# Performance work log

Hardware: AMD Instinct MI355X
Metric: run time of the kernel (lower is better)

## Reference

```python
import jax, jax.numpy as jnp
import numpy as np

B, V, C, M, CM, D, OUT = 16, 16, 64, 32, 16, 128, 600
VOCAB = {"cond": 4000, "proc": 2000, "drug": 600, "lab_item": 700, "lab_value": 2000, "inj_item": 400, "inj_value": 2000}


def _gru(x, Wih, Whh, bih, bhh):
    """Batch-first torch-style GRU. x: [N,T,D] -> (outputs [N,T,D], h_T [N,D])."""
    Dh = Whh.shape[1]

    def step(h, xt):
        gi = xt @ Wih.T + bih
        gh = h @ Whh.T + bhh
        ir, iz, ig = jnp.split(gi, 3, axis=-1)
        hr, hz, hg = jnp.split(gh, 3, axis=-1)
        r = jax.nn.sigmoid(ir + hr)
        z = jax.nn.sigmoid(iz + hz)
        n = jnp.tanh(ig + r * hg)
        h = (1.0 - z) * n + z * h
        return h, h

    h0 = jnp.zeros((x.shape[0], Dh), x.dtype)
    hT, ys = jax.lax.scan(step, h0, jnp.swapaxes(x, 0, 1))
    return jnp.swapaxes(ys, 0, 1), hT


def _hetero_mp(feats, Wself, Wmsg):
    """Heterogeneous message passing over node types on the fully-connected
    monitor<->visit-feature bipartite pattern: each node type combines a self
    transform with a transformed mean of the other node types, then ReLU.
    feats: list of [N,D]; Wself/Wmsg: [T,D,D]."""
    stacked = jnp.stack(feats)  # [T,N,D]
    total = jnp.sum(stacked, axis=0)
    T = stacked.shape[0]
    outs = []
    for t in range(T):
        others = (total - stacked[t]) / (T - 1)
        outs.append(jax.nn.relu(stacked[t] @ Wself[t] + others @ Wmsg[t]))
    return outs


def _forward(codes_cond, codes_proc, codes_drug, codes_lab_item, codes_lab_value,
             codes_inj_item, codes_inj_value, weight, age,
             emb_cond, emb_proc, emb_drug, emb_lab_item, emb_lab_value,
             emb_inj_item, emb_inj_value,
             mgru_Wih, mgru_Whh, mgru_bih, mgru_bhh,
             vgru_Wih, vgru_Whh, vgru_bih, vgru_bhh,
             gnn_Wself, gnn_Wmsg,
             fc_weight_W, fc_weight_b, fc_age_W, fc_age_b,
             fc_patient_W, fc_patient_b):
    # ---- visit-event features: embedding lookup + sum-pool over codes ----
    vis = {}
    for k, codes, emb in (("cond", codes_cond, emb_cond),
                          ("proc", codes_proc, emb_proc),
                          ("drug", codes_drug, emb_drug)):
        vis[k] = jnp.sum(emb[codes], axis=2)  # [B,V,D]
    visit_keys = ("cond", "proc", "drug")

    # ---- monitor-event pairs: (item * value) embeddings, GNN, two-level GRU ----
    pairs = (
        (codes_lab_item, codes_lab_value, emb_lab_item, emb_lab_value, "lab_item", (0, 2, 3, 4)),
        (codes_inj_item, codes_inj_value, emb_inj_item, emb_inj_value, "inj_item", (1, 2, 3, 4)),
    )
    hid = {}
    for p, (ci, cv, ei, ev, ikey, gidx) in enumerate(pairs):
        mon = jnp.sum(ei[ci] * ev[cv], axis=3)  # [B,V,M,D]
        feats = [mon.reshape(-1, D)]  # monitor node type, [B*V*M, D]
        for k in visit_keys:  # visit features repeated across monitors
            feats.append(jnp.broadcast_to(vis[k][:, :, None, :], (B, V, M, D)).reshape(-1, D))
        outs = _hetero_mp(feats, gnn_Wself[p], gnn_Wmsg[p])
        for t, k in enumerate((ikey,) + visit_keys):
            g = gidx[t]
            # monitor-level GRU over the M monitors of each visit
            o, _ = _gru(outs[t].reshape(B * V, M, D), mgru_Wih[g], mgru_Whh[g], mgru_bih[g], mgru_bhh[g])
            last = o[:, -1, :].reshape(B, V, D)  # last monitor state per visit
            # visit-level GRU (source uses visit_gru[feature_key1] for all keys)
            _, h = _gru(last, vgru_Wih[p], vgru_Whh[p], vgru_bih[p], vgru_bhh[p])
            hid[k] = h if k not in hid else hid[k] + h

    # ---- weight / age scalar features ----
    for k, x, W, b, vi in (("weight", weight, fc_weight_W, fc_weight_b, 2),
                           ("age", age, fc_age_W, fc_age_b, 3)):
        mask = (x != 0.0)[..., None]  # [B,V,1]
        xe = (x[..., None] * W[:, 0] + b) * mask  # Linear(1->D) then zero-mask
        _, h = _gru(xe, vgru_Wih[vi], vgru_Whh[vi], vgru_bih[vi], vgru_bhh[vi])
        hid[k] = h

    # ---- concat in dict-insertion order, then ReLU + Linear head ----
    pe = jnp.concatenate([hid["lab_item"], hid["cond"], hid["proc"], hid["drug"],
                          hid["inj_item"], hid["weight"], hid["age"]], axis=-1)  # [B, 7D]
    return jax.nn.relu(pe) @ fc_patient_W.T + fc_patient_b  # [B, OUT]


def setup_inputs() -> dict:
    key = jax.random.key(0)
    ks = iter(jax.random.split(key, 64))

    def nrm(shape, s=0.1):
        return (jax.random.normal(next(ks), shape) * s).astype(jnp.float32)

    def emb_table(vsz):
        t = nrm((vsz, D), 1.0)
        return t.at[0].set(0.0)  # padding_idx=0 row is zero

    inp = {}
    inp["codes_cond"] = jax.random.randint(next(ks), (B, V, C), 0, VOCAB["cond"], dtype=jnp.int32)
    inp["codes_proc"] = jax.random.randint(next(ks), (B, V, C), 0, VOCAB["proc"], dtype=jnp.int32)
    inp["codes_drug"] = jax.random.randint(next(ks), (B, V, C), 0, VOCAB["drug"], dtype=jnp.int32)
    inp["codes_lab_item"] = jax.random.randint(next(ks), (B, V, M, CM), 0, VOCAB["lab_item"], dtype=jnp.int32)
    inp["codes_lab_value"] = jax.random.randint(next(ks), (B, V, M, CM), 0, VOCAB["lab_value"], dtype=jnp.int32)
    inp["codes_inj_item"] = jax.random.randint(next(ks), (B, V, M, CM), 0, VOCAB["inj_item"], dtype=jnp.int32)
    inp["codes_inj_value"] = jax.random.randint(next(ks), (B, V, M, CM), 0, VOCAB["inj_value"], dtype=jnp.int32)
    inp["weight"] = jax.random.uniform(next(ks), (B, V), minval=0.1, maxval=1.0, dtype=jnp.float32)
    inp["age"] = jax.random.uniform(next(ks), (B, V), minval=0.1, maxval=1.0, dtype=jnp.float32)
    inp["emb_cond"] = emb_table(VOCAB["cond"])
    inp["emb_proc"] = emb_table(VOCAB["proc"])
    inp["emb_drug"] = emb_table(VOCAB["drug"])
    inp["emb_lab_item"] = emb_table(VOCAB["lab_item"])
    inp["emb_lab_value"] = emb_table(VOCAB["lab_value"])
    inp["emb_inj_item"] = emb_table(VOCAB["inj_item"])
    inp["emb_inj_value"] = emb_table(VOCAB["inj_value"])
    inp["mgru_Wih"] = nrm((5, 3 * D, D))
    inp["mgru_Whh"] = nrm((5, 3 * D, D))
    inp["mgru_bih"] = nrm((5, 3 * D))
    inp["mgru_bhh"] = nrm((5, 3 * D))
    inp["vgru_Wih"] = nrm((4, 3 * D, D))
    inp["vgru_Whh"] = nrm((4, 3 * D, D))
    inp["vgru_bih"] = nrm((4, 3 * D))
    inp["vgru_bhh"] = nrm((4, 3 * D))
    inp["gnn_Wself"] = nrm((2, 4, D, D))
    inp["gnn_Wmsg"] = nrm((2, 4, D, D))
    inp["fc_weight_W"] = nrm((D, 1))
    inp["fc_weight_b"] = nrm((D,))
    inp["fc_age_W"] = nrm((D, 1))
    inp["fc_age_b"] = nrm((D,))
    inp["fc_patient_W"] = nrm((OUT, 7 * D))
    inp["fc_patient_b"] = nrm((OUT,))
    return inp


def reference(codes_cond, codes_proc, codes_drug, codes_lab_item, codes_lab_value,
              codes_inj_item, codes_inj_value, weight, age,
              emb_cond, emb_proc, emb_drug, emb_lab_item, emb_lab_value,
              emb_inj_item, emb_inj_value,
              mgru_Wih, mgru_Whh, mgru_bih, mgru_bhh,
              vgru_Wih, vgru_Whh, vgru_bih, vgru_bhh,
              gnn_Wself, gnn_Wmsg,
              fc_weight_W, fc_weight_b, fc_age_W, fc_age_b,
              fc_patient_W, fc_patient_b):
    return _forward(codes_cond, codes_proc, codes_drug, codes_lab_item, codes_lab_value,
                    codes_inj_item, codes_inj_value, weight, age,
                    emb_cond, emb_proc, emb_drug, emb_lab_item, emb_lab_value,
                    emb_inj_item, emb_inj_value,
                    mgru_Wih, mgru_Whh, mgru_bih, mgru_bhh,
                    vgru_Wih, vgru_Whh, vgru_bih, vgru_bhh,
                    gnn_Wself, gnn_Wmsg,
                    fc_weight_W, fc_weight_b, fc_age_W, fc_age_b,
                    fc_patient_W, fc_patient_b)
```

## Files before the change

kernel.cpp:

```cpp
#include <hip/hip_runtime.h>
#include <math.h>

#define B_   16
#define V_   16
#define C_   64
#define M_   32
#define CM_  16
#define D_   128
#define OUT_ 600
#define NSEQ 256
#define NROW 8192

typedef __attribute__((ext_vector_type(8))) short bf16x8;
typedef __attribute__((ext_vector_type(4))) short bf16x4;
typedef __attribute__((ext_vector_type(4))) float f32x4;

__device__ __forceinline__ unsigned short f2bf(float x) {
  union { float f; unsigned u; } v; v.f = x;
  unsigned r = v.u + 0x7fff + ((v.u >> 16) & 1);
  return (unsigned short)(r >> 16);
}
__device__ __forceinline__ float bf2f(short s) {
  union { unsigned u; float f; } v;
  v.u = ((unsigned)(unsigned short)s) << 16;
  return v.f;
}
__device__ __forceinline__ float fsig(float x)  { return __fdividef(1.f, 1.f + __expf(-x)); }
__device__ __forceinline__ float ftanh(float x) { return 1.f - 2.f*__fdividef(1.f, __expf(2.f*x) + 1.f); }

constexpr int OFF_VIS   = 0;
constexpr int OFF_VISB  = 98304;
constexpr int OFF_MONB  = 147456;
constexpr int OFF_TOTB  = 1196032;
constexpr int OFF_W12T  = 2244608;
constexpr int OFF_WIHB  = 2375680;
constexpr int OFF_WIHTV = 2498560;
constexpr int OFF_XE    = 2695168;
constexpr int OFF_GI    = 2760704;
constexpr int OFF_LAST  = 27926528;
constexpr int OFF_VH    = 29171712;

__global__ __launch_bounds__(256) void k_prepvis(
    const float* __restrict__ Wself, const float* __restrict__ Wmsg,
    const float* __restrict__ mWih,  const float* __restrict__ vWih,
    const float* __restrict__ wgt,   const float* __restrict__ age,
    const float* __restrict__ fwW,   const float* __restrict__ fwB,
    const float* __restrict__ faW,   const float* __restrict__ faB,
    const int* __restrict__ cc, const int* __restrict__ cp, const int* __restrict__ cd,
    const float* __restrict__ ec, const float* __restrict__ ep, const float* __restrict__ ed,
    short* __restrict__ w12t, short* __restrict__ wihb,
    float* __restrict__ wihTv, float* __restrict__ xe,
    float* __restrict__ vis, short* __restrict__ visb)
{
  int bx = blockIdx.x, tid = threadIdx.x;
  if (bx < 1024) {
    int lin = bx*256 + tid;
    int pt = lin >> 15, rem = lin & 32767;
    int n = rem >> 8, k = rem & 255;
    float v;
    if (k < 128) v = Wself[pt*16384 + k*128 + n] - Wmsg[pt*16384 + k*128 + n]*(1.f/3.f);
    else         v = Wmsg[pt*16384 + (k-128)*128 + n]*(1.f/3.f);
    w12t[lin] = (short)f2bf(v);
  } else if (bx < 1984) {
    int lin = (bx-1024)*256 + tid;
    wihb[lin] = (short)f2bf(mWih[lin]);
  } else if (bx < 2752) {
    int lin = (bx-1984)*256 + tid;
    int g = lin / 49152, rem2 = lin % 49152;
    int k = rem2 / 384, j = rem2 % 384;
    wihTv[lin] = vWih[g*49152 + j*128 + k];
  } else if (bx < 3008) {
    int lin = (bx-2752)*256 + tid;
    int which = lin >> 15, rem2 = lin & 32767;
    int n = rem2 >> 7, d = rem2 & 127;
    float x  = which ? age[n] : wgt[n];
    float Wv = which ? faW[d] : fwW[d];
    float bb = which ? faB[d] : fwB[d];
    xe[lin] = (x != 0.0f) ? (x*Wv + bb) : 0.0f;
  } else {
    int idx = (bx-3008)*256 + tid;
    int type = idx >> 15;
    int r = idx & 32767;
    int bv = r >> 7, d = r & 127;
    const int*   codes = (type==0) ? cc : (type==1) ? cp : cd;
    const float* emb   = (type==0) ? ec : (type==1) ? ep : ed;
    float acc = 0.f;
    for (int c = 0; c < C_; ++c) {
      int code = codes[bv*C_ + c];
      acc += emb[code*D_ + d];
    }
    vis [(type*NSEQ + bv)*D_ + d] = acc;
    visb[(type*NSEQ + bv)*D_ + d] = (short)f2bf(acc);
  }
}

__global__ __launch_bounds__(128) void k_mon(
    const int* __restrict__ cli, const int* __restrict__ clv,
    const int* __restrict__ cii, const int* __restrict__ civ,
    const float* __restrict__ eli, const float* __restrict__ elv,
    const float* __restrict__ eii, const float* __restrict__ eiv,
    const float* __restrict__ vis,
    short* __restrict__ monb, short* __restrict__ totb)
{
  int p   = blockIdx.x >> 13;
  int bvm = blockIdx.x & 8191;
  int d   = threadIdx.x;
  const int* ci = p ? cii : cli;  const int* cv = p ? civ : clv;
  const float* ei = p ? eii : eli; const float* ev = p ? eiv : elv;
  float acc = 0.f;
  #pragma unroll
  for (int c = 0; c < CM_; ++c) {
    int iv = ci[bvm*CM_ + c];
    int vv = cv[bvm*CM_ + c];
    acc += ei[iv*D_ + d] * ev[vv*D_ + d];
  }
  int bv = bvm >> 5;
  float vsum = vis[bv*D_ + d] + vis[(NSEQ + bv)*D_ + d] + vis[(2*NSEQ + bv)*D_ + d];
  monb[(p*NROW + bvm)*D_ + d] = (short)f2bf(acc);
  totb[(p*NROW + bvm)*D_ + d] = (short)f2bf(acc + vsum);
}

__global__ __launch_bounds__(256, 4) void k_gg(
    const short* __restrict__ monb, const short* __restrict__ totb,
    const short* __restrict__ visb, const short* __restrict__ w12t,
    const short* __restrict__ wihb, const float* __restrict__ mbih,
    short* __restrict__ gi)
{
  const int pt = blockIdx.x >> 6;
  const int rb = blockIdx.x & 63;
  const int p = pt >> 2, t = pt & 3;
  const int g = (pt % 4 == 0) ? (pt / 4) : (pt % 4 + 1);
  const int row0 = rb * 128;
  const int tid = threadIdx.x;
  const int w = tid >> 6, lane = tid & 63;
  const int c = lane & 15, q = lane >> 4;

  __shared__ short smem[2*128*72];
  short (*Xs)[72]  = (short(*)[72])smem;
  short (*Ws)[72]  = (short(*)[72])(smem + 128*72);
  short (*Ys)[136] = (short(*)[136])smem;
  float (*giS)[68] = (float(*)[68])smem;

  const int rowL = tid >> 1, kc = tid & 1;
  const int rowG = row0 + rowL;
  const int bv = rowG >> 5;
  const int mg = w >> 1, ng = w & 1;

  f32x4 acc1[4][4];
  #pragma unroll
  for (int mi = 0; mi < 4; ++mi)
    #pragma unroll
    for (int ni = 0; ni < 4; ++ni) acc1[mi][ni] = (f32x4){0.f,0.f,0.f,0.f};

  const short* featp = (t == 0) ? (monb + ((size_t)p*NROW + rowG)*128)
                                : (visb + ((size_t)(t-1)*NSEQ + bv)*128);
  const short* totp  = totb + ((size_t)p*NROW + rowG)*128;
  const short* wrow  = w12t + ((size_t)pt*128 + rowL)*256;

  #pragma unroll 1
  for (int ks = 0; ks < 4; ++ks) {
    __syncthreads();
    int kg = ks*64 + kc*32;
    const short* srcX = (kg < 128) ? (featp + kg) : (totp + (kg - 128));
    const short* srcW = wrow + kg;
    short* dX = &Xs[rowL][kc*32];
    short* dW = &Ws[rowL][kc*32];
    #pragma unroll
    for (int i = 0; i < 4; ++i) {
      *(bf16x8*)(dX + 8*i) = *(const bf16x8*)(srcX + 8*i);
      *(bf16x8*)(dW + 8*i) = *(const bf16x8*)(srcW + 8*i);
    }
    __syncthreads();
    #pragma unroll
    for (int kk = 0; kk < 2; ++kk) {
      bf16x8 af[4], bfr[4];
      #pragma unroll
      for (int mi = 0; mi < 4; ++mi)
        af[mi] = *(const bf16x8*)&Xs[(mg*4+mi)*16 + c][kk*32 + q*8];
      #pragma unroll
      for (int ni = 0; ni < 4; ++ni)
        bfr[ni] = *(const bf16x8*)&Ws[(ng*4+ni)*16 + c][kk*32 + q*8];
      #pragma unroll
      for (int mi = 0; mi < 4; ++mi)
        #pragma unroll
        for (int ni = 0; ni < 4; ++ni)
          acc1[mi][ni] = __builtin_amdgcn_mfma_f32_16x16x32_bf16(af[mi], bfr[ni], acc1[mi][ni], 0, 0, 0);
    }
  }
  __syncthreads();

  #pragma unroll
  for (int mi = 0; mi < 4; ++mi)
    #pragma unroll
    for (int ni = 0; ni < 4; ++ni)
      #pragma unroll
      for (int reg = 0; reg < 4; ++reg)
        Ys[(mg*4+mi)*16 + q*4 + reg][(ng*4+ni)*16 + c] =
            (short)f2bf(fmaxf(acc1[mi][ni][reg], 0.f));
  __syncthreads();

  bf16x8 Af[2][4];
  #pragma unroll
  for (int mi = 0; mi < 2; ++mi)
    #pragma unroll
    for (int kt = 0; kt < 4; ++kt)
      Af[mi][kt] = *(const bf16x8*)&Ys[(w*2+mi)*16 + c][kt*32 + q*8];

  float bihv[24];
  #pragma unroll
  for (int nt = 0; nt < 24; ++nt)
    bihv[nt] = mbih[g*384 + nt*16 + c];

  short* gslab = gi + (((size_t)pt*64 + rb)*32)*384*4;
  #pragma unroll 1
  for (int cn = 0; cn < 6; ++cn) {
    f32x4 acc2[2][4];
    #pragma unroll
    for (int mi = 0; mi < 2; ++mi)
      #pragma unroll
      for (int ni = 0; ni < 4; ++ni) acc2[mi][ni] = (f32x4){0.f,0.f,0.f,0.f};
    #pragma unroll
    for (int ni = 0; ni < 4; ++ni) {
      int n = (cn*4 + ni)*16 + c;
      const short* bp_ = wihb + ((size_t)g*384 + n)*128 + q*8;
      #pragma unroll
      for (int kt = 0; kt < 4; ++kt) {
        bf16x8 bfr = *(const bf16x8*)(bp_ + kt*32);
        #pragma unroll
        for (int mi = 0; mi < 2; ++mi)
          acc2[mi][ni] = __builtin_amdgcn_mfma_f32_16x16x32_bf16(Af[mi][kt], bfr, acc2[mi][ni], 0, 0, 0);
      }
    }
    __syncthreads();
    #pragma unroll
    for (int mi = 0; mi < 2; ++mi)
      #pragma unroll
      for (int ni = 0; ni < 4; ++ni) {
        float bia = bihv[cn*4+ni];
        #pragma unroll
        for (int reg = 0; reg < 4; ++reg)
          giS[(w*2+mi)*16 + q*4 + reg][ni*16 + c] = acc2[mi][ni][reg] + bia;
      }
    __syncthreads();
    #pragma unroll
    for (int k = 0; k < 8; ++k) {
      int o4 = tid + k*256;
      int m = o4 >> 6, colL = o4 & 63;
      bf16x4 v;
      v[0] = (short)f2bf(giS[m][colL]);
      v[1] = (short)f2bf(giS[32+m][colL]);
      v[2] = (short)f2bf(giS[64+m][colL]);
      v[3] = (short)f2bf(giS[96+m][colL]);
      *(bf16x4*)&gslab[((size_t)m*384 + cn*64 + colL)*4] = v;
    }
  }
}

__global__ __launch_bounds__(512, 1) void k_mgru(
    const short* __restrict__ gi, const float* __restrict__ mWhh,
    const float* __restrict__ mbhh, float* __restrict__ last)
{
  const int run = blockIdx.x >> 5, grp = blockIdx.x & 31;
  const int g = (run % 4 == 0) ? (run / 4) : (run % 4 + 1);
  const int tid = threadIdx.x;
  const int w = tid >> 6;
  const int lane = tid & 63;
  const int c = lane & 15, q = lane >> 4;

  __shared__ short hb[2][4][16][40];
  for (int idx = tid; idx < 2*4*16*40; idx += 512)
    ((short*)hb)[idx] = 0;

  const int jh = w*16 + c;

  bf16x8 bfrag[3][4];
  #pragma unroll
  for (int gate = 0; gate < 3; ++gate) {
    const float* wp = mWhh + ((size_t)g*384 + gate*128 + jh)*128 + q*8;
    #pragma unroll
    for (int kt = 0; kt < 4; ++kt) {
      float4 lo = *(const float4*)(wp + kt*32);
      float4 hi = *(const float4*)(wp + kt*32 + 4);
      bf16x8 t;
      t[0]=(short)f2bf(lo.x); t[1]=(short)f2bf(lo.y); t[2]=(short)f2bf(lo.z); t[3]=(short)f2bf(lo.w);
      t[4]=(short)f2bf(hi.x); t[5]=(short)f2bf(hi.y); t[6]=(short)f2bf(hi.z); t[7]=(short)f2bf(hi.w);
      bfrag[gate][kt] = t;
    }
  }
  float bh_[3];
  #pragma unroll
  for (int gate = 0; gate < 3; ++gate)
    bh_[gate] = mbhh[g*384 + gate*128 + jh];

  float hf[4] = {0.f,0.f,0.f,0.f};
  const short* gib = gi + (((size_t)run*64 + grp*2 + q)*32)*384*4;
  const bool act = (lane < 32);

  bf16x4 gA[3], gB[3];
  if (act) {
    #pragma unroll
    for (int gate = 0; gate < 3; ++gate)
      gA[gate] = *(const bf16x4*)&gib[(size_t)(0*384 + gate*128 + jh)*4];
  }
  __syncthreads();

  auto dostep = [&](int m, bf16x4 (&gcur)[3], bf16x4 (&gnext)[3]) {
    const int cur = m & 1, nxt = cur ^ 1;
    bf16x8 a[4];
    #pragma unroll
    for (int kt = 0; kt < 4; ++kt)
      a[kt] = *(const bf16x8*)&hb[cur][kt][c][q*8];

    f32x4 acc[3];
    #pragma unroll
    for (int gate = 0; gate < 3; ++gate) {
      f32x4 t = {0.f,0.f,0.f,0.f};
      #pragma unroll
      for (int kt = 0; kt < 4; ++kt)
        t = __builtin_amdgcn_mfma_f32_16x16x32_bf16(a[kt], bfrag[gate][kt], t, 0, 0, 0);
      acc[gate] = t;
    }

    if (act && m < 31) {
      #pragma unroll
      for (int gate = 0; gate < 3; ++gate)
        gnext[gate] = *(const bf16x4*)&gib[(size_t)((m+1)*384 + gate*128 + jh)*4];
    }

    if (act) {
      const int kt = jh >> 5, kk = jh & 31;
      #pragma unroll
      for (int reg = 0; reg < 4; ++reg) {
        int row = q*4 + reg;
        float g0 = bf2f(gcur[0][reg]);
        float g1 = bf2f(gcur[1][reg]);
        float g2 = bf2f(gcur[2][reg]);
        float rr = fsig(acc[0][reg] + bh_[0] + g0);
        float zz = fsig(acc[1][reg] + bh_[1] + g1);
        float nn = ftanh(g2 + rr*(acc[2][reg] + bh_[2]));
        float hnew = (1.f - zz)*nn + zz*hf[reg];
        hf[reg] = hnew;
        hb[nxt][kt][row][kk] = (short)f2bf(hnew);
      }
    }
    __syncthreads();
  };

  #pragma unroll 1
  for (int m2 = 0; m2 < 16; ++m2) {
    dostep(2*m2,     gA, gB);
    dostep(2*m2 + 1, gB, gA);
  }

  if (act) {
    #pragma unroll
    for (int reg = 0; reg < 4; ++reg)
      last[(run*NSEQ + grp*8 + q*4 + reg)*D_ + jh] = hf[reg];
  }
}

__global__ __launch_bounds__(768) void k_vgru(
    const float* __restrict__ last, const float* __restrict__ xe,
    const float* __restrict__ wihTv, const float* __restrict__ vbih,
    const float* __restrict__ vWhh, const float* __restrict__ vbhh,
    float* __restrict__ vh)
{
  int run = blockIdx.x >> 4, b = blockIdx.x & 15;
  int tid = threadIdx.x;
  int vidx = (run < 4) ? 0 : (run < 8) ? 1 : (run - 6);

  __shared__ float Xs[16][128];
  __shared__ float giL[16*384];
  __shared__ __align__(16) float hsv[128];
  __shared__ float gh[384];

  const float* X = (run < 8) ? (last + ((size_t)run*NSEQ + b*16)*D_)
                             : (xe + ((size_t)(run-8)*NSEQ + b*16)*D_);
  for (int idx = tid; idx < 2048; idx += 768)
    ((float*)Xs)[idx] = X[idx];
  if (tid < 128) hsv[tid] = 0.f;
  __syncthreads();

  {
    int half = (tid >= 384) ? 1 : 0;
    int j = tid - half*384;
    float accv[8];
    float bias = vbih[vidx*384 + j];
    #pragma unroll
    for (int s = 0; s < 8; ++s) accv[s] = bias;
    const float* W = wihTv + vidx*49152 + j;
    #pragma unroll 4
    for (int k = 0; k < 128; ++k) {
      float wv = W[k*384];
      #pragma unroll
      for (int s = 0; s < 8; ++s) accv[s] += Xs[half*8 + s][k] * wv;
    }
    #pragma unroll
    for (int s = 0; s < 8; ++s)
      giL[(half*8 + s)*384 + j] = accv[s];
  }

  int j = tid >> 1, kh = tid & 1;
  float w[64];
  const float4* wrow = (const float4*)(vWhh + (vidx*384 + j)*128 + kh*64);
  #pragma unroll
  for (int k4 = 0; k4 < 16; ++k4) {
    float4 t4 = wrow[k4];
    w[4*k4] = t4.x; w[4*k4+1] = t4.y; w[4*k4+2] = t4.z; w[4*k4+3] = t4.w;
  }
  float bj = vbhh[vidx*384 + j];
  __syncthreads();

  #pragma unroll 1
  for (int v = 0; v < 16; ++v) {
    const float4* h4 = (const float4*)(hsv + kh*64);
    float p0 = 0.f, p1 = 0.f;
    #pragma unroll
    for (int k4 = 0; k4 < 8; ++k4) {
      float4 u0 = h4[k4], u1 = h4[k4+8];
      p0 += w[4*k4   ]*u0.x + w[4*k4+1 ]*u0.y + w[4*k4+2 ]*u0.z + w[4*k4+3 ]*u0.w;
      p1 += w[4*k4+32]*u1.x + w[4*k4+33]*u1.y + w[4*k4+34]*u1.z + w[4*k4+35]*u1.w;
    }
    float part = p0 + p1;
    part += __shfl_xor(part, 1);
    if (kh == 0) gh[j] = bj + ((j < 256) ? giL[v*384 + j] : 0.f) + part;
    __syncthreads();
    if (tid < 128) {
      float r = fsig(gh[tid]);
      float z = fsig(gh[tid+128]);
      float gin = giL[v*384 + 256 + tid];
      float n = ftanh(gin + r*gh[tid+256]);
      hsv[tid] = (1.f - z)*n + z*hsv[tid];
    }
    __syncthreads();
  }
  if (tid < 128) vh[(run*16 + b)*D_ + tid] = hsv[tid];
}

__global__ __launch_bounds__(256) void k_head(
    const float* __restrict__ vh, const float* __restrict__ Wp,
    const float* __restrict__ bp, float* __restrict__ out)
{
  const int o = blockIdx.x;
  const int tid = threadIdx.x;
  const int b = tid & 15, kc = tid >> 4;
  const int a1[7] = {0,1,2,3,4,8,9};
  const int a2[7] = {-1,5,6,7,-1,-1,-1};
  const float4* wb = (const float4*)(Wp + (size_t)o*896 + kc*56);
  float acc = 0.f;
  #pragma unroll
  for (int i = 0; i < 14; ++i) {
    int cc2 = kc*56 + i*4;
    int s = cc2 >> 7, d0 = cc2 & 127;
    float4 a = *(const float4*)(vh + (a1[s]*16 + b)*D_ + d0);
    int s2 = a2[s];
    if (s2 >= 0) {
      float4 a2v = *(const float4*)(vh + (s2*16 + b)*D_ + d0);
      a.x += a2v.x; a.y += a2v.y; a.z += a2v.z; a.w += a2v.w;
    }
    a.x = fmaxf(a.x, 0.f); a.y = fmaxf(a.y, 0.f);
    a.z = fmaxf(a.z, 0.f); a.w = fmaxf(a.w, 0.f);
    float4 ww = wb[i];
    acc += a.x*ww.x + a.y*ww.y + a.z*ww.z + a.w*ww.w;
  }
  __shared__ float red[16][17];
  red[kc][b] = acc;
  __syncthreads();
  if (tid < 16) {
    float s = 0.f;
    #pragma unroll
    for (int k = 0; k < 16; ++k) s += red[k][tid];
    out[tid*OUT_ + o] = s + bp[o];
  }
}

extern "C" void kernel_launch(void* const* d_in, const int* in_sizes, int n_in,
                              void* d_out, int out_size, void* d_ws, size_t ws_size,
                              hipStream_t stream)
{
  (void)in_sizes; (void)n_in; (void)out_size; (void)ws_size;
  const int*   cc   = (const int*)  d_in[0];
  const int*   cp   = (const int*)  d_in[1];
  const int*   cd   = (const int*)  d_in[2];
  const int*   cli  = (const int*)  d_in[3];
  const int*   clv  = (const int*)  d_in[4];
  const int*   cii  = (const int*)  d_in[5];
  const int*   civ  = (const int*)  d_in[6];
  const float* wgt  = (const float*)d_in[7];
  const float* age  = (const float*)d_in[8];
  const float* ec   = (const float*)d_in[9];
  const float* ep   = (const float*)d_in[10];
  const float* ed   = (const float*)d_in[11];
  const float* eli  = (const float*)d_in[12];
  const float* elv  = (const float*)d_in[13];
  const float* eii  = (const float*)d_in[14];
  const float* eiv  = (const float*)d_in[15];
  const float* mWih = (const float*)d_in[16];
  const float* mWhh = (const float*)d_in[17];
  const float* mbih = (const float*)d_in[18];
  const float* mbhh = (const float*)d_in[19];
  const float* vWih = (const float*)d_in[20];
  const float* vWhh = (const float*)d_in[21];
  const float* vbih = (const float*)d_in[22];
  const float* vbhh = (const float*)d_in[23];
  const float* Wself= (const float*)d_in[24];
  const float* Wmsg = (const float*)d_in[25];
  const float* fwW  = (const float*)d_in[26];
  const float* fwB  = (const float*)d_in[27];
  const float* faW  = (const float*)d_in[28];
  const float* faB  = (const float*)d_in[29];
  const float* Wp   = (const float*)d_in[30];
  const float* bp   = (const float*)d_in[31];
  float* out = (float*)d_out;
  float* ws  = (float*)d_ws;

  float* vis   = ws + OFF_VIS;
  short* visb  = (short*)(ws + OFF_VISB);
  short* monb  = (short*)(ws + OFF_MONB);
  short* totb  = (short*)(ws + OFF_TOTB);
  short* w12t  = (short*)(ws + OFF_W12T);
  short* wihb  = (short*)(ws + OFF_WIHB);
  float* wihTv = ws + OFF_WIHTV;
  float* xe    = ws + OFF_XE;
  short* gi    = (short*)(ws + OFF_GI);
  float* last  = ws + OFF_LAST;
  float* vh    = ws + OFF_VH;

  k_prepvis<<<3392, 256, 0, stream>>>(Wself, Wmsg, mWih, vWih, wgt, age,
                                      fwW, fwB, faW, faB,
                                      cc, cp, cd, ec, ep, ed,
                                      w12t, wihb, wihTv, xe, vis, visb);
  k_mon <<<16384, 128, 0, stream>>>(cli, clv, cii, civ, eli, elv, eii, eiv,
                                    vis, monb, totb);
  k_gg  <<<512, 256, 0, stream>>>(monb, totb, visb, w12t, wihb, mbih, gi);
  k_mgru<<<256, 512, 0, stream>>>(gi, mWhh, mbhh, last);
  k_vgru<<<160, 768, 0, stream>>>(last, xe, wihTv, vbih, vWhh, vbhh, vh);
  k_head<<<600, 256, 0, stream>>>(vh, Wp, bp, out);
}
```

Baseline: 276.7 us.

## Split k_gg row tiles in half to double block count

```diff
diff --git a/kernel.cpp b/kernel.cpp
--- a/kernel.cpp
+++ b/kernel.cpp
@@ -13,6 +13,7 @@
 
 typedef __attribute__((ext_vector_type(8))) short bf16x8;
 typedef __attribute__((ext_vector_type(4))) short bf16x4;
+typedef __attribute__((ext_vector_type(2))) short bf16x2;
 typedef __attribute__((ext_vector_type(4))) float f32x4;
 
 __device__ __forceinline__ unsigned short f2bf(float x) {
@@ -126,99 +127,85 @@
     const short* __restrict__ wihb, const float* __restrict__ mbih,
     short* __restrict__ gi)
 {
-  const int pt = blockIdx.x >> 6;
-  const int rb = blockIdx.x & 63;
+  const int bx = blockIdx.x;
+  const int half = bx >> 9;
+  const int pt = (bx & 511) >> 6;
+  const int rb = bx & 63;
   const int p = pt >> 2, t = pt & 3;
   const int g = (pt % 4 == 0) ? (pt / 4) : (pt % 4 + 1);
-  const int row0 = rb * 128;
+  const int row0 = rb * 128 + half * 64;
   const int tid = threadIdx.x;
   const int w = tid >> 6, lane = tid & 63;
   const int c = lane & 15, q = lane >> 4;
 
-  __shared__ short smem[2*128*72];
+  __shared__ short smem[64*72 + 128*72];
   short (*Xs)[72]  = (short(*)[72])smem;
-  short (*Ws)[72]  = (short(*)[72])(smem + 128*72);
+  short (*Ws)[72]  = (short(*)[72])(smem + 64*72);
   short (*Ys)[136] = (short(*)[136])smem;
   float (*giS)[68] = (float(*)[68])smem;
 
-  const int rowL = tid >> 1, kc = tid & 1;
+  const int rowL = tid >> 2;
+  const int kq   = tid & 3;
   const int rowG = row0 + rowL;
-  const int bv = rowG >> 5;
-  const int mg = w >> 1, ng = w & 1;
-
-  f32x4 acc1[4][4];
-  #pragma unroll
-  for (int mi = 0; mi < 4; ++mi)
-    #pragma unroll
-    for (int ni = 0; ni < 4; ++ni) acc1[mi][ni] = (f32x4){0.f,0.f,0.f,0.f};
+  const int bv   = rowG >> 5;
+
+  f32x4 acc1[8];
+  #pragma unroll
+  for (int ni = 0; ni < 8; ++ni) acc1[ni] = (f32x4){0.f,0.f,0.f,0.f};
 
   const short* featp = (t == 0) ? (monb + ((size_t)p*NROW + rowG)*128)
                                 : (visb + ((size_t)(t-1)*NSEQ + bv)*128);
   const short* totp  = totb + ((size_t)p*NROW + rowG)*128;
-  const short* wrow  = w12t + ((size_t)pt*128 + rowL)*256;
+  const short* wrow  = w12t + ((size_t)pt*128 + (tid>>1))*256;
 
   #pragma unroll 1
   for (int ks = 0; ks < 4; ++ks) {
     __syncthreads();
-    int kg = ks*64 + kc*32;
+    int kg = ks*64 + kq*16;
     const short* srcX = (kg < 128) ? (featp + kg) : (totp + (kg - 128));
-    const short* srcW = wrow + kg;
-    short* dX = &Xs[rowL][kc*32];
-    short* dW = &Ws[rowL][kc*32];
-    #pragma unroll
-    for (int i = 0; i < 4; ++i) {
-      *(bf16x8*)(dX + 8*i) = *(const bf16x8*)(srcX + 8*i);
+    *(bf16x8*)&Xs[rowL][kq*16]     = *(const bf16x8*)(srcX);
+    *(bf16x8*)&Xs[rowL][kq*16 + 8] = *(const bf16x8*)(srcX + 8);
+    const short* srcW = wrow + ks*64 + (tid&1)*32;
+    short* dW = &Ws[tid>>1][(tid&1)*32];
+    #pragma unroll
+    for (int i = 0; i < 4; ++i)
       *(bf16x8*)(dW + 8*i) = *(const bf16x8*)(srcW + 8*i);
-    }
     __syncthreads();
     #pragma unroll
     for (int kk = 0; kk < 2; ++kk) {
-      bf16x8 af[4], bfr[4];
-      #pragma unroll
-      for (int mi = 0; mi < 4; ++mi)
-        af[mi] = *(const bf16x8*)&Xs[(mg*4+mi)*16 + c][kk*32 + q*8];
-      #pragma unroll
-      for (int ni = 0; ni < 4; ++ni)
-        bfr[ni] = *(const bf16x8*)&Ws[(ng*4+ni)*16 + c][kk*32 + q*8];
-      #pragma unroll
-      for (int mi = 0; mi < 4; ++mi)
-        #pragma unroll
-        for (int ni = 0; ni < 4; ++ni)
-          acc1[mi][ni] = __builtin_amdgcn_mfma_f32_16x16x32_bf16(af[mi], bfr[ni], acc1[mi][ni], 0, 0, 0);
+      bf16x8 af = *(const bf16x8*)&Xs[w*16 + c][kk*32 + q*8];
+      #pragma unroll
+      for (int ni = 0; ni < 8; ++ni) {
+        bf16x8 bfr = *(const bf16x8*)&Ws[ni*16 + c][kk*32 + q*8];
+        acc1[ni] = __builtin_amdgcn_mfma_f32_16x16x32_bf16(af, bfr, acc1[ni], 0, 0, 0);
+      }
     }
   }
   __syncthreads();
 
   #pragma unroll
-  for (int mi = 0; mi < 4; ++mi)
-    #pragma unroll
-    for (int ni = 0; ni < 4; ++ni)
-      #pragma unroll
-      for (int reg = 0; reg < 4; ++reg)
-        Ys[(mg*4+mi)*16 + q*4 + reg][(ng*4+ni)*16 + c] =
-            (short)f2bf(fmaxf(acc1[mi][ni][reg], 0.f));
+  for (int ni = 0; ni < 8; ++ni)
+    #pragma unroll
+    for (int reg = 0; reg < 4; ++reg)
+      Ys[w*16 + q*4 + reg][ni*16 + c] = (short)f2bf(fmaxf(acc1[ni][reg], 0.f));
   __syncthreads();
 
-  bf16x8 Af[2][4];
-  #pragma unroll
-  for (int mi = 0; mi < 2; ++mi)
-    #pragma unroll
-    for (int kt = 0; kt < 4; ++kt)
-      Af[mi][kt] = *(const bf16x8*)&Ys[(w*2+mi)*16 + c][kt*32 + q*8];
+  bf16x8 Af[4];
+  #pragma unroll
+  for (int kt = 0; kt < 4; ++kt)
+    Af[kt] = *(const bf16x8*)&Ys[w*16 + c][kt*32 + q*8];
 
   float bihv[24];
   #pragma unroll
   for (int nt = 0; nt < 24; ++nt)
     bihv[nt] = mbih[g*384 + nt*16 + c];
 
-  short* gslab = gi + (((size_t)pt*64 + rb)*32)*384*4;
+  short* gslab = gi + (((size_t)pt*64 + rb)*32)*384*4 + half*2;
   #pragma unroll 1
   for (int cn = 0; cn < 6; ++cn) {
-    f32x4 acc2[2][4];
-    #pragma unroll
-    for (int mi = 0; mi < 2; ++mi)
-      #pragma unroll
-      for (int ni = 0; ni < 4; ++ni) acc2[mi][ni] = (f32x4){0.f,0.f,0.f,0.f};
+    f32x4 acc2[4];
+    #pragma unroll
+    for (int ni = 0; ni < 4; ++ni) acc2[ni] = (f32x4){0.f,0.f,0.f,0.f};
     #pragma unroll
     for (int ni = 0; ni < 4; ++ni) {
       int n = (cn*4 + ni)*16 + c;
@@ -226,32 +213,26 @@
       #pragma unroll
       for (int kt = 0; kt < 4; ++kt) {
         bf16x8 bfr = *(const bf16x8*)(bp_ + kt*32);
-        #pragma unroll
-        for (int mi = 0; mi < 2; ++mi)
-          acc2[mi][ni] = __builtin_amdgcn_mfma_f32_16x16x32_bf16(Af[mi][kt], bfr, acc2[mi][ni], 0, 0, 0);
+        acc2[ni] = __builtin_amdgcn_mfma_f32_16x16x32_bf16(Af[kt], bfr, acc2[ni], 0, 0, 0);
       }
     }
     __syncthreads();
     #pragma unroll
-    for (int mi = 0; mi < 2; ++mi)
-      #pragma unroll
-      for (int ni = 0; ni < 4; ++ni) {
-        float bia = bihv[cn*4+ni];
-        #pragma unroll
-        for (int reg = 0; reg < 4; ++reg)
-          giS[(w*2+mi)*16 + q*4 + reg][ni*16 + c] = acc2[mi][ni][reg] + bia;
-      }
-    __syncthreads();
-    #pragma unroll
-    for (int k = 0; k < 8; ++k) {
-      int o4 = tid + k*256;
-      int m = o4 >> 6, colL = o4 & 63;
-      bf16x4 v;
+    for (int ni = 0; ni < 4; ++ni) {
+      float bia = bihv[cn*4+ni];
+      #pragma unroll
+      for (int reg = 0; reg < 4; ++reg)
+        giS[w*16 + q*4 + reg][ni*16 + c] = acc2[ni][reg] + bia;
+    }
+    __syncthreads();
+    #pragma unroll
+    for (int k2 = 0; k2 < 8; ++k2) {
+      int o = tid + k2*256;
+      int m = o >> 6, colL = o & 63;
+      bf16x2 v;
       v[0] = (short)f2bf(giS[m][colL]);
       v[1] = (short)f2bf(giS[32+m][colL]);
-      v[2] = (short)f2bf(giS[64+m][colL]);
-      v[3] = (short)f2bf(giS[96+m][colL]);
-      *(bf16x4*)&gslab[((size_t)m*384 + cn*64 + colL)*4] = v;
+      *(bf16x2*)&gslab[((size_t)m*384 + cn*64 + colL)*4] = v;
     }
   }
 }
@@ -532,7 +513,7 @@
                                       w12t, wihb, wihTv, xe, vis, visb);
   k_mon <<<16384, 128, 0, stream>>>(cli, clv, cii, civ, eli, elv, eii, eiv,
                                     vis, monb, totb);
-  k_gg  <<<512, 256, 0, stream>>>(monb, totb, visb, w12t, wihb, mbih, gi);
+  k_gg  <<<1024, 256, 0, stream>>>(monb, totb, visb, w12t, wihb, mbih, gi);
   k_mgru<<<256, 512, 0, stream>>>(gi, mWhh, mbhh, last);
   k_vgru<<<160, 768, 0, stream>>>(last, xe, wihTv, vbih, vWhh, vbhh, vh);
   k_head<<<600, 256, 0, stream>>>(vh, Wp, bp, out);
```

New measurement: 302.1 us. 1.09x slower.

## Fuse monitor pooling into prep kernel and compute total features inside GEMM

Applied to the files above, without the earlier changes.

```diff
diff --git a/kernel.cpp b/kernel.cpp
--- a/kernel.cpp
+++ b/kernel.cpp
@@ -31,14 +31,13 @@
 constexpr int OFF_VIS   = 0;
 constexpr int OFF_VISB  = 98304;
 constexpr int OFF_MONB  = 147456;
-constexpr int OFF_TOTB  = 1196032;
-constexpr int OFF_W12T  = 2244608;
-constexpr int OFF_WIHB  = 2375680;
-constexpr int OFF_WIHTV = 2498560;
-constexpr int OFF_XE    = 2695168;
-constexpr int OFF_GI    = 2760704;
-constexpr int OFF_LAST  = 27926528;
-constexpr int OFF_VH    = 29171712;
+constexpr int OFF_W12T  = 1196032;
+constexpr int OFF_WIHB  = 1327104;
+constexpr int OFF_WIHTV = 1449984;
+constexpr int OFF_XE    = 1646592;
+constexpr int OFF_GI    = 1712128;
+constexpr int OFF_LAST  = 14295040;
+constexpr int OFF_VH    = 14557184;
 
 __global__ __launch_bounds__(256) void k_prepvis(
     const float* __restrict__ Wself, const float* __restrict__ Wmsg,
@@ -48,9 +47,14 @@
     const float* __restrict__ faW,   const float* __restrict__ faB,
     const int* __restrict__ cc, const int* __restrict__ cp, const int* __restrict__ cd,
     const float* __restrict__ ec, const float* __restrict__ ep, const float* __restrict__ ed,
+    const int* __restrict__ cli, const int* __restrict__ clv,
+    const int* __restrict__ cii, const int* __restrict__ civ,
+    const float* __restrict__ eli, const float* __restrict__ elv,
+    const float* __restrict__ eii, const float* __restrict__ eiv,
     short* __restrict__ w12t, short* __restrict__ wihb,
     float* __restrict__ wihTv, float* __restrict__ xe,
-    float* __restrict__ vis, short* __restrict__ visb)
+    float* __restrict__ vis, short* __restrict__ visb,
+    short* __restrict__ monb)
 {
   int bx = blockIdx.x, tid = threadIdx.x;
   if (bx < 1024) {
@@ -77,7 +81,7 @@
     float Wv = which ? faW[d] : fwW[d];
     float bb = which ? faB[d] : fwB[d];
     xe[lin] = (x != 0.0f) ? (x*Wv + bb) : 0.0f;
-  } else {
+  } else if (bx < 3392) {
     int idx = (bx-3008)*256 + tid;
     int type = idx >> 15;
     int r = idx & 32767;
@@ -91,37 +95,25 @@
     }
     vis [(type*NSEQ + bv)*D_ + d] = acc;
     visb[(type*NSEQ + bv)*D_ + d] = (short)f2bf(acc);
-  }
-}
-
-__global__ __launch_bounds__(128) void k_mon(
-    const int* __restrict__ cli, const int* __restrict__ clv,
-    const int* __restrict__ cii, const int* __restrict__ civ,
-    const float* __restrict__ eli, const float* __restrict__ elv,
-    const float* __restrict__ eii, const float* __restrict__ eiv,
-    const float* __restrict__ vis,
-    short* __restrict__ monb, short* __restrict__ totb)
-{
-  int p   = blockIdx.x >> 13;
-  int bvm = blockIdx.x & 8191;
-  int d   = threadIdx.x;
-  const int* ci = p ? cii : cli;  const int* cv = p ? civ : clv;
-  const float* ei = p ? eii : eli; const float* ev = p ? eiv : elv;
-  float acc = 0.f;
-  #pragma unroll
-  for (int c = 0; c < CM_; ++c) {
-    int iv = ci[bvm*CM_ + c];
-    int vv = cv[bvm*CM_ + c];
-    acc += ei[iv*D_ + d] * ev[vv*D_ + d];
-  }
-  int bv = bvm >> 5;
-  float vsum = vis[bv*D_ + d] + vis[(NSEQ + bv)*D_ + d] + vis[(2*NSEQ + bv)*D_ + d];
-  monb[(p*NROW + bvm)*D_ + d] = (short)f2bf(acc);
-  totb[(p*NROW + bvm)*D_ + d] = (short)f2bf(acc + vsum);
+  } else {
+    int r = (bx-3392)*2 + (tid >> 7);
+    int p = r >> 13, bvm = r & 8191;
+    int d = tid & 127;
+    const int* ci = p ? cii : cli;  const int* cv = p ? civ : clv;
+    const float* ei = p ? eii : eli; const float* ev = p ? eiv : elv;
+    float acc = 0.f;
+    #pragma unroll
+    for (int c = 0; c < CM_; ++c) {
+      int iv = ci[bvm*CM_ + c];
+      int vv = cv[bvm*CM_ + c];
+      acc += ei[iv*D_ + d] * ev[vv*D_ + d];
+    }
+    monb[((size_t)p*NROW + bvm)*D_ + d] = (short)f2bf(acc);
+  }
 }
 
 __global__ __launch_bounds__(256, 4) void k_gg(
-    const short* __restrict__ monb, const short* __restrict__ totb,
+    const short* __restrict__ monb, const float* __restrict__ vis,
     const short* __restrict__ visb, const short* __restrict__ w12t,
     const short* __restrict__ wihb, const float* __restrict__ mbih,
     short* __restrict__ gi)
@@ -152,24 +144,42 @@
     #pragma unroll
     for (int ni = 0; ni < 4; ++ni) acc1[mi][ni] = (f32x4){0.f,0.f,0.f,0.f};
 
-  const short* featp = (t == 0) ? (monb + ((size_t)p*NROW + rowG)*128)
+  const short* monp  = monb + ((size_t)p*NROW + rowG)*128;
+  const short* featp = (t == 0) ? monp
                                 : (visb + ((size_t)(t-1)*NSEQ + bv)*128);
-  const short* totp  = totb + ((size_t)p*NROW + rowG)*128;
+  const float* vA = vis + (size_t)(0*NSEQ + bv)*D_;
+  const float* vB = vis + (size_t)(1*NSEQ + bv)*D_;
+  const float* vC = vis + (size_t)(2*NSEQ + bv)*D_;
   const short* wrow  = w12t + ((size_t)pt*128 + rowL)*256;
 
   #pragma unroll 1
   for (int ks = 0; ks < 4; ++ks) {
     __syncthreads();
     int kg = ks*64 + kc*32;
-    const short* srcX = (kg < 128) ? (featp + kg) : (totp + (kg - 128));
+    short* dX = &Xs[rowL][kc*32];
+    if (kg < 128) {
+      const short* srcX = featp + kg;
+      #pragma unroll
+      for (int i = 0; i < 4; ++i)
+        *(bf16x8*)(dX + 8*i) = *(const bf16x8*)(srcX + 8*i);
+    } else {
+      int k2 = kg - 128;
+      const short* mrow = monp + k2;
+      #pragma unroll
+      for (int i = 0; i < 4; ++i) {
+        bf16x8 m8 = *(const bf16x8*)(mrow + 8*i);
+        bf16x8 t8;
+        #pragma unroll
+        for (int j = 0; j < 8; ++j)
+          t8[j] = (short)f2bf(bf2f(m8[j]) + vA[k2+8*i+j] + vB[k2+8*i+j] + vC[k2+8*i+j]);
+        *(bf16x8*)(dX + 8*i) = t8;
+      }
+    }
     const short* srcW = wrow + kg;
-    short* dX = &Xs[rowL][kc*32];
     short* dW = &Ws[rowL][kc*32];
     #pragma unroll
-    for (int i = 0; i < 4; ++i) {
-      *(bf16x8*)(dX + 8*i) = *(const bf16x8*)(srcX + 8*i);
+    for (int i = 0; i < 4; ++i)
       *(bf16x8*)(dW + 8*i) = *(const bf16x8*)(srcW + 8*i);
-    }
     __syncthreads();
     #pragma unroll
     for (int kk = 0; kk < 2; ++kk) {
@@ -517,7 +527,6 @@
   float* vis   = ws + OFF_VIS;
   short* visb  = (short*)(ws + OFF_VISB);
   short* monb  = (short*)(ws + OFF_MONB);
-  short* totb  = (short*)(ws + OFF_TOTB);
   short* w12t  = (short*)(ws + OFF_W12T);
   short* wihb  = (short*)(ws + OFF_WIHB);
   float* wihTv = ws + OFF_WIHTV;
@@ -526,13 +535,12 @@
   float* last  = ws + OFF_LAST;
   float* vh    = ws + OFF_VH;
 
-  k_prepvis<<<3392, 256, 0, stream>>>(Wself, Wmsg, mWih, vWih, wgt, age,
-                                      fwW, fwB, faW, faB,
-                                      cc, cp, cd, ec, ep, ed,
-                                      w12t, wihb, wihTv, xe, vis, visb);
-  k_mon <<<16384, 128, 0, stream>>>(cli, clv, cii, civ, eli, elv, eii, eiv,
-                                    vis, monb, totb);
-  k_gg  <<<512, 256, 0, stream>>>(monb, totb, visb, w12t, wihb, mbih, gi);
+  k_prepvis<<<11584, 256, 0, stream>>>(Wself, Wmsg, mWih, vWih, wgt, age,
+                                       fwW, fwB, faW, faB,
+                                       cc, cp, cd, ec, ep, ed,
+                                       cli, clv, cii, civ, eli, elv, eii, eiv,
+                                       w12t, wihb, wihTv, xe, vis, visb, monb);
+  k_gg  <<<512, 256, 0, stream>>>(monb, vis, visb, w12t, wihb, mbih, gi);
   k_mgru<<<256, 512, 0, stream>>>(gi, mWhh, mbhh, last);
   k_vgru<<<160, 768, 0, stream>>>(last, xe, wihTv, vbih, vWhh, vbhh, vh);
   k_head<<<600, 256, 0, stream>>>(vh, Wp, bp, out);
```

Result: slower. 286.6 us (+3.6%).
